# Optimization experiments

Hardware: AMD Instinct MI355X
Metric: run time of the kernel (lower is better)

## Reference

```python
import jax, jax.numpy as jnp
import numpy as np

B, T, D_IN, H, D = 4, 4096, 1024, 16, 64


def setup_inputs() -> dict:
    key = jax.random.key(0)
    k1, k2, k3 = jax.random.split(key, 3)
    inputs = jax.random.normal(k1, (B, T, D_IN), dtype=jnp.float32)
    kv_kernel = jax.random.normal(k2, (D_IN, H, D, 2), dtype=jnp.float32) * (1.0 / np.sqrt(D_IN))
    q_kernel = jax.random.normal(k3, (H, D), dtype=jnp.float32) * (1.0 / np.sqrt(D))
    return {"inputs": inputs, "kv_kernel": kv_kernel, "q_kernel": q_kernel}


def _associate(a, b):
    # Online-softmax combine on packed tuples [m(1), u(1), w(D)] along last axis.
    ma, ua, wa = a[..., :1], a[..., 1:2], a[..., 2:]
    mb, ub, wb = b[..., :1], b[..., 1:2], b[..., 2:]
    m = jnp.maximum(ma, mb)
    ea = jnp.exp(ma - m)
    eb = jnp.exp(mb - m)
    u = ua * ea + ub * eb
    w = wa * ea + wb * eb
    return jnp.concatenate([m, u, w], axis=-1)


def reference(inputs, kv_kernel, q_kernel):
    # inputs: (B,T,D_in); kv_kernel: (D_in,H,D,2); q_kernel: (H,D)
    kv = jnp.einsum('bti,ihdk->bthdk', inputs, kv_kernel)
    kv = jax.nn.relu(kv)  # activation; dropout disabled (inference)
    k = kv[..., 0]  # (B,T,H,D)
    v = kv[..., 1]  # (B,T,H,D)
    st = jnp.einsum('hd,bthd->bth', q_kernel, k)[..., None]  # (B,T,H,1)
    u_init = jnp.ones_like(st)  # exp(s - m) with m = s
    elems = jnp.concatenate([st, u_init, v], axis=-1)  # (B,T,H,D+2)
    o = jax.lax.associative_scan(_associate, elems, axis=1)
    c = o[..., 1:2]  # running denominator
    a = o[..., 2:]   # running numerator (B,T,H,D)
    h = a / c
    # concat_heads=False -> sum over heads
    return jnp.sum(h, axis=-2)  # (B,T,D)
```

## Files before the change

kernel.cpp:

```cpp
#include <hip/hip_runtime.h>
#include <hip/hip_bf16.h>
#include <math.h>

#define B_   4
#define T_   4096
#define DIN_ 1024
#define H_   16
#define D_   64
#define M_   (B_*T_)
#define N_   (H_*D_*2)
#define K_   DIN_
#define C_   64
#define CL_  (T_/C_)

typedef unsigned short u16;
typedef __attribute__((ext_vector_type(8))) short short8_t;
typedef __attribute__((ext_vector_type(4))) float float4_t;

__device__ __forceinline__ u16 f2bf(float f) {
  unsigned int x = __float_as_uint(f);
  x += 0x7fffu + ((x >> 16) & 1u);
  return (u16)(x >> 16);
}
__device__ __forceinline__ float bf2f(unsigned int u) {
  return __uint_as_float((u & 0xffffu) << 16);
}
__device__ __forceinline__ unsigned pk_bf16(float x, float y) {
  float2 f; f.x = x; f.y = y;
  union { __hip_bfloat162 h2; unsigned u; } c;
  c.h2 = __float22bfloat162_rn(f);
  return c.u;
}

__device__ __forceinline__ void g2l16(const u16* g, u16* l) {
  __builtin_amdgcn_global_load_lds(
      (const __attribute__((address_space(1))) void*)g,
      (__attribute__((address_space(3))) void*)l, 16, 0, 0);
}

__global__ __launch_bounds__(256)
void prep(const float* __restrict__ inputs, const float* __restrict__ kvk,
          u16* __restrict__ aB, u16* __restrict__ wBt) {
  __shared__ float tile[32][33];
  int bid = blockIdx.x;
  int tid = threadIdx.x;
  if (bid < 8192) {
    int i = bid * 256 + tid;
    const float4* src = (const float4*)inputs;
    float4 a = src[2*i], b = src[2*i+1];
    uint4 o;
    o.x = pk_bf16(a.x, a.y);
    o.y = pk_bf16(a.z, a.w);
    o.z = pk_bf16(b.x, b.y);
    o.w = pk_bf16(b.z, b.w);
    ((uint4*)aB)[i] = o;
  } else {
    int b2 = bid - 8192;
    int kb = (b2 & 31) * 32;
    int nb = (b2 >> 5) * 32;
    int r  = tid >> 3;
    int c4 = (tid & 7) * 4;
    float4 v = *(const float4*)&kvk[(size_t)(kb + r) * N_ + nb + c4];
    tile[r][c4+0] = v.x; tile[r][c4+1] = v.y; tile[r][c4+2] = v.z; tile[r][c4+3] = v.w;
    __syncthreads();
    uint2 o;
    o.x = pk_bf16(tile[c4+0][r], tile[c4+1][r]);
    o.y = pk_bf16(tile[c4+2][r], tile[c4+3][r]);
    *(uint2*)&wBt[(size_t)(nb + r) * K_ + kb + c4] = o;
  }
}


#define FENCE asm volatile("" ::: "memory")
#define KBAR do { FENCE; __builtin_amdgcn_s_barrier(); FENCE; } while (0)

#define STAGE_A(P, KT, CC) do { \
  g2l16(gA + ((size_t)((CC)*64      ) * K_ + (KT)*64), lds + (P)*16384 +        (CC)*4096 + wv*512); \
  g2l16(gA + ((size_t)((CC)*64 + 128) * K_ + (KT)*64), lds + (P)*16384 + 8192 + (CC)*4096 + wv*512); \
} while (0)

#define STAGE_B(P, KT, HH) do { \
  g2l16(gB + ((size_t)((HH)*128     ) * K_ + (KT)*64), lds + 32768 + (P)*16384 + (HH)*8192 +        wv*512); \
  g2l16(gB + ((size_t)((HH)*128 + 64) * K_ + (KT)*64), lds + 32768 + (P)*16384 + (HH)*8192 + 4096 + wv*512); \
} while (0)

#define READ_A(P, MH) do { _Pragma("unroll") \
  for (int il_ = 0; il_ < 4; ++il_) { \
    const int o_ = (P)*16384 + aBase + (MH)*4096 + il_*1024; \
    af[il_][0] = *(const short8_t*)&lds[o_ + s0]; \
    af[il_][1] = *(const short8_t*)&lds[o_ + s1]; \
  } } while (0)

#define READ_B(P, NH) do { _Pragma("unroll") \
  for (int jl_ = 0; jl_ < 2; ++jl_) { \
    const int o_ = (P)*16384 + (NH)*8192 + bBase + jl_*1024; \
    bfr[NH][jl_][0] = *(const short8_t*)&lds[o_ + s0]; \
    bfr[NH][jl_][1] = *(const short8_t*)&lds[o_ + s1]; \
  } } while (0)

#define MFMA_Q(MH, NH) do { \
  __builtin_amdgcn_s_setprio(1); \
  _Pragma("unroll") for (int kk_ = 0; kk_ < 2; ++kk_) \
  _Pragma("unroll") for (int il_ = 0; il_ < 4; ++il_) \
  _Pragma("unroll") for (int jl_ = 0; jl_ < 2; ++jl_) \
    acc[(MH)*4+il_][(NH)*2+jl_] = __builtin_amdgcn_mfma_f32_16x16x32_bf16( \
        af[il_][kk_], bfr[NH][jl_][kk_], acc[(MH)*4+il_][(NH)*2+jl_], 0, 0, 0); \
  __builtin_amdgcn_s_setprio(0); \
} while (0)

__global__ __launch_bounds__(512, 2)
void gemm_kv(const u16* __restrict__ A, const u16* __restrict__ Bt,
             const float* __restrict__ q,
             float* __restrict__ pbuf, u16* __restrict__ vbuf,
             float* __restrict__ aggU, float* __restrict__ aggW) {
  extern __shared__ __align__(16) char smem[];
  u16* lds = (u16*)smem;

  const int tid  = threadIdx.x;
  const int wv   = tid >> 6;
  const int lane = tid & 63;
  const int quad = lane >> 4;
  const int l16  = lane & 15;
  const int wr   = wv >> 2;
  const int wc   = wv & 3;

  const int g  = blockIdx.x;
  const int wg = (g & 7) * 64 + (g >> 3);
  const int nt = wg & 7;
  const int mt = wg >> 3;
  const int bm = mt * 256;
  const int bn = nt * 256;

  const int tr   = tid >> 3;
  const int gran = tid & 7;
  const u16* gA = A  + (size_t)(bm + tr) * K_ + ((gran ^ (tr & 7)) * 8);
  const u16* gB = Bt + (size_t)(bn + tr) * K_ + ((gran ^ (tr & 7)) * 8);

  const int s0 = ((quad    ) ^ (l16 & 7)) * 8;
  const int s1 = ((quad + 4) ^ (l16 & 7)) * 8;
  const int aBase = wr * 8192 + l16 * 64;
  const int bBase = 32768 + wc * 2048 + l16 * 64;

  float4_t acc[8][4] = {};
  short8_t af[4][2];
  short8_t bfr[2][2][2];

  STAGE_A(0, 0, 0); STAGE_A(0, 0, 1);
  STAGE_B(0, 0, 0); STAGE_B(0, 0, 1);
  STAGE_A(1, 1, 0); STAGE_B(1, 1, 0);
  asm volatile("s_waitcnt vmcnt(4)" ::: "memory");
  KBAR;

#pragma unroll 1
  for (int it = 0; it < 8; ++it) {
    const int kt1 = 2*it + 1, kt2 = 2*it + 2, kt3 = 2*it + 3;
    const bool more = (it < 7);
    READ_A(0, 0); READ_B(0, 0);
    STAGE_A(1, kt1, 1);
    KBAR;
    MFMA_Q(0, 0);
    KBAR;
    READ_B(0, 1);
    STAGE_B(1, kt1, 1);
    KBAR;
    MFMA_Q(0, 1);
    KBAR;
    READ_A(0, 1);
    if (more) STAGE_A(0, kt2, 0);
    KBAR;
    MFMA_Q(1, 0);
    KBAR;
    if (more) STAGE_B(0, kt2, 0);
    KBAR;
    MFMA_Q(1, 1);
    if (more) asm volatile("s_waitcnt vmcnt(4)" ::: "memory");
    else      asm volatile("s_waitcnt vmcnt(0)" ::: "memory");
    KBAR;
    READ_A(1, 0); READ_B(1, 0);
    if (more) STAGE_A(0, kt2, 1);
    KBAR;
    MFMA_Q(0, 0);
    KBAR;
    READ_B(1, 1);
    if (more) STAGE_B(0, kt2, 1);
    KBAR;
    MFMA_Q(0, 1);
    KBAR;
    READ_A(1, 1);
    if (more) STAGE_A(1, kt3, 0);
    KBAR;
    MFMA_Q(1, 0);
    KBAR;
    if (more) STAGE_B(1, kt3, 0);
    KBAR;
    MFMA_Q(1, 1);
    if (more) asm volatile("s_waitcnt vmcnt(4)" ::: "memory");
    KBAR;
  }

  u16*   vtile = (u16*)smem;
  float* sred  = (float*)(smem + 73728);
  float* pS    = (float*)(smem + 108544);

  float qv[2][2];
#pragma unroll
  for (int nh = 0; nh < 2; ++nh)
#pragma unroll
    for (int jl = 0; jl < 2; ++jl)
      qv[nh][jl] = q[nt*128 + nh*64 + wc*16 + jl*8 + (l16 >> 1)];

#pragma unroll
  for (int nh = 0; nh < 2; ++nh) {
#pragma unroll
    for (int i = 0; i < 8; ++i) {
#pragma unroll
      for (int r = 0; r < 4; ++r) {
        const int t = wr*128 + i*16 + quad*4 + r;
        const float x0 = fmaxf(acc[i][nh*2+0][r], 0.f);
        const float x1 = fmaxf(acc[i][nh*2+1][r], 0.f);
        if (l16 & 1) {
          const int d0 = (wc*32 + l16) >> 1;
          vtile[(nh*256 + t)*72 + d0    ] = f2bf(x0);
          vtile[(nh*256 + t)*72 + d0 + 8] = f2bf(x1);
        }
        float ps = qv[nh][0]*x0 + qv[nh][1]*x1;
        ps += __shfl_xor(ps, 2);
        if ((l16 & 3) == 0)
          sred[(nh*256 + t)*17 + wc*4 + (l16 >> 2)] = ps;
      }
    }
  }
  __syncthreads();

  const int b  = mt >> 4;
  const int t0 = (mt & 15) * 256;
  {
    const int hh = tid >> 8;
    const int t  = tid & 255;
    float s = 0.f;
#pragma unroll
    for (int k = 0; k < 16; ++k) s += sred[(hh*256 + t)*17 + k];
    float p = __expf(fminf(fmaxf(s, -60.f), 60.f));
    pS[hh*256 + t] = p;
    pbuf[(size_t)(b*H_ + nt*2 + hh) * T_ + t0 + t] = p;
    float u = p;
#pragma unroll
    for (int off = 32; off; off >>= 1) u += __shfl_down(u, off);
    if (lane == 0) {
      const int ch = (tid >> 6) & 3;
      aggU[(b*H_ + nt*2 + hh)*C_ + (mt & 15)*4 + ch] = u;
    }
  }
  __syncthreads();

  if (l16 & 1) {
    float Wv[2][2][2] = {};
#pragma unroll
    for (int nh = 0; nh < 2; ++nh)
#pragma unroll
      for (int i = 0; i < 8; ++i)
#pragma unroll
        for (int r = 0; r < 4; ++r) {
          const int t = wr*128 + i*16 + quad*4 + r;
          const float p = pS[nh*256 + t];
          Wv[nh][i>>2][0] += p * fmaxf(acc[i][nh*2+0][r], 0.f);
          Wv[nh][i>>2][1] += p * fmaxf(acc[i][nh*2+1][r], 0.f);
        }
#pragma unroll
    for (int nh = 0; nh < 2; ++nh)
#pragma unroll
      for (int c2 = 0; c2 < 2; ++c2)
#pragma unroll
        for (int jl = 0; jl < 2; ++jl) {
          float w = Wv[nh][c2][jl];
          w += __shfl_xor(w, 16);
          w += __shfl_xor(w, 32);
          if (quad == 0) {
            const int blk = (b*H_ + nt*2 + nh)*C_ + (mt & 15)*4 + wr*2 + c2;
            aggW[(size_t)blk * D_ + wc*16 + jl*8 + (l16 >> 1)] = w;
          }
        }
  }
  {
    const int rr = tid >> 3;
    const int d0 = (tid & 7) * 8;
#pragma unroll
    for (int k2 = 0; k2 < 8; ++k2) {
      const int row = rr + 64*k2;
      const int hh  = row >> 8;
      const int t   = row & 255;
      uint4 val = *(const uint4*)&vtile[(hh*256 + t)*72 + d0];
      *(uint4*)&vbuf[((size_t)(b*H_ + nt*2 + hh) * T_ + t0 + t) * D_ + d0] = val;
    }
  }
}

__global__ __launch_bounds__(1024)
void scan_pass3(const u16* __restrict__ vbuf, const float* __restrict__ pbuf,
                const float* __restrict__ aggU, const float* __restrict__ aggW,
                float* __restrict__ out) {
  __shared__ float pS[H_][CL_];
  __shared__ float wbuf[H_][8][D_ + 1];
  int bc = blockIdx.x;
  int b  = bc >> 6;
  int c  = bc & (C_ - 1);
  int tid  = threadIdx.x;
  int h    = tid >> 6;
  int lane = tid & 63;
  int bh   = b * H_ + h;
  int t0   = c * CL_;

  pS[h][lane] = pbuf[(size_t)bh * T_ + t0 + lane];

  float U = 0.f, W = 0.f;
  for (int j = 0; j < c; ++j) {
    int idx = bh * C_ + j;
    U += aggU[idx];
    W += aggW[(size_t)idx * D_ + lane];
  }
  __syncthreads();

  const u16* vp = vbuf + ((size_t)bh * T_ + t0) * D_ + lane;
  for (int gg = 0; gg < 8; ++gg) {
#pragma unroll
    for (int ii = 0; ii < 8; ++ii) {
      int i = gg * 8 + ii;
      float p = pS[h][i];
      float v = bf2f(vp[i * D_]);
      U += p;
      W += p * v;
      wbuf[h][ii][lane] = __fdividef(W, U);
    }
    __syncthreads();
    if (tid < 512) {
      int ii = tid >> 6, dd = tid & 63;
      float acc = 0.f;
#pragma unroll
      for (int hh = 0; hh < H_; ++hh) acc += wbuf[hh][ii][dd];
      out[((size_t)b * T_ + t0 + gg*8 + ii) * D_ + dd] = acc;
    }
    __syncthreads();
  }
}

extern "C" void kernel_launch(void* const* d_in, const int* in_sizes, int n_in,
                              void* d_out, int out_size, void* d_ws, size_t ws_size,
                              hipStream_t stream) {
  const float* inputs = (const float*)d_in[0];
  const float* kvk    = (const float*)d_in[1];
  const float* qk     = (const float*)d_in[2];
  float* out = (float*)d_out;
  char* ws = (char*)d_ws;

  u16*   aB   = (u16*)ws;
  u16*   wBt  = (u16*)(ws + 33554432);
  u16*   vb   = (u16*)(ws + 37748736);
  float* pb   = (float*)(ws + 71303168);
  float* aggU = (float*)(ws + 72351744);
  float* aggW = (float*)(ws + 72368128);

  prep<<<10240, 256, 0, stream>>>(inputs, kvk, aB, wBt);
  gemm_kv<<<2048 / 4, 512, 131072, stream>>>(aB, wBt, qk, pb, vb, aggU, aggW);
  scan_pass3<<<B_*C_, 1024, 0, stream>>>(vb, pb, aggU, aggW, out);
}
```

Baseline: 205.4 us.

## Restructure KV GEMM to 16 waves with K=32 triple-buffered LDS pipeline

Reworks the fused KV GEMM from 8 waves holding 128x64 register tiles, double-buffered with K=64 steps, to 16 waves per block each holding a 64x64 tile. The main loop now uses K=32 steps with a three-slot LDS ring and one stage per phase. LDS shrinks to 96KB and the launch becomes 1024 threads, and the epilogue is adapted to the new wave-to-tile mapping. The goal is more waves to hide latency and a simpler pipeline, at the cost of more barriers per unit of K and less register reuse per wave.

```diff
diff --git a/kernel.cpp b/kernel.cpp
--- a/kernel.cpp
+++ b/kernel.cpp
@@ -74,41 +74,35 @@
 #define FENCE asm volatile("" ::: "memory")
 #define KBAR do { FENCE; __builtin_amdgcn_s_barrier(); FENCE; } while (0)
 
-#define STAGE_A(P, KT, CC) do { \
-  g2l16(gA + ((size_t)((CC)*64      ) * K_ + (KT)*64), lds + (P)*16384 +        (CC)*4096 + wv*512); \
-  g2l16(gA + ((size_t)((CC)*64 + 128) * K_ + (KT)*64), lds + (P)*16384 + 8192 + (CC)*4096 + wv*512); \
+#define READS(PAR) do { _Pragma("unroll") \
+  for (int i_ = 0; i_ < 4; ++i_) \
+    af[i_] = *(const short8_t*)&lds[(PAR)*8192 + aBase + i_*512]; \
+  _Pragma("unroll") \
+  for (int j_ = 0; j_ < 4; ++j_) \
+    bfq[j_] = *(const short8_t*)&lds[(PAR)*8192 + bBase + j_*512]; \
 } while (0)
 
-#define STAGE_B(P, KT, HH) do { \
-  g2l16(gB + ((size_t)((HH)*128     ) * K_ + (KT)*64), lds + 32768 + (P)*16384 + (HH)*8192 +        wv*512); \
-  g2l16(gB + ((size_t)((HH)*128 + 64) * K_ + (KT)*64), lds + 32768 + (P)*16384 + (HH)*8192 + 4096 + wv*512); \
-} while (0)
-
-#define READ_A(P, MH) do { _Pragma("unroll") \
-  for (int il_ = 0; il_ < 4; ++il_) { \
-    const int o_ = (P)*16384 + aBase + (MH)*4096 + il_*1024; \
-    af[il_][0] = *(const short8_t*)&lds[o_ + s0]; \
-    af[il_][1] = *(const short8_t*)&lds[o_ + s1]; \
-  } } while (0)
-
-#define READ_B(P, NH) do { _Pragma("unroll") \
-  for (int jl_ = 0; jl_ < 2; ++jl_) { \
-    const int o_ = (P)*16384 + (NH)*8192 + bBase + jl_*1024; \
-    bfr[NH][jl_][0] = *(const short8_t*)&lds[o_ + s0]; \
-    bfr[NH][jl_][1] = *(const short8_t*)&lds[o_ + s1]; \
-  } } while (0)
-
-#define MFMA_Q(MH, NH) do { \
+#define MFMAS do { \
   __builtin_amdgcn_s_setprio(1); \
-  _Pragma("unroll") for (int kk_ = 0; kk_ < 2; ++kk_) \
-  _Pragma("unroll") for (int il_ = 0; il_ < 4; ++il_) \
-  _Pragma("unroll") for (int jl_ = 0; jl_ < 2; ++jl_) \
-    acc[(MH)*4+il_][(NH)*2+jl_] = __builtin_amdgcn_mfma_f32_16x16x32_bf16( \
-        af[il_][kk_], bfr[NH][jl_][kk_], acc[(MH)*4+il_][(NH)*2+jl_], 0, 0, 0); \
+  _Pragma("unroll") for (int i_ = 0; i_ < 4; ++i_) \
+  _Pragma("unroll") for (int j_ = 0; j_ < 4; ++j_) \
+    acc[i_][j_] = __builtin_amdgcn_mfma_f32_16x16x32_bf16( \
+        af[i_], bfq[j_], acc[i_][j_], 0, 0, 0); \
   __builtin_amdgcn_s_setprio(0); \
 } while (0)
 
-__global__ __launch_bounds__(512, 2)
+#define PHASE(PAR, PAR2, KT) do { \
+  short8_t af[4], bfq[4]; \
+  READS(PAR); \
+  g2l16(gA + ((KT)+2)*32, lds +         (PAR2)*8192 + wv*512); \
+  g2l16(gB + ((KT)+2)*32, lds + 24576 + (PAR2)*8192 + wv*512); \
+  KBAR; \
+  MFMAS; \
+  asm volatile("s_waitcnt vmcnt(2)" ::: "memory"); \
+  KBAR; \
+} while (0)
+
+__global__ __launch_bounds__(1024)
 void gemm_kv(const u16* __restrict__ A, const u16* __restrict__ Bt,
              const float* __restrict__ q,
              float* __restrict__ pbuf, u16* __restrict__ vbuf,
@@ -121,8 +115,8 @@
   const int lane = tid & 63;
   const int quad = lane >> 4;
   const int l16  = lane & 15;
-  const int wr   = wv >> 2;
-  const int wc   = wv & 3;
+  const int wr2  = wv >> 2;
+  const int wc2  = wv & 3;
 
   const int g  = blockIdx.x;
   const int wg = (g & 7) * 64 + (g >> 3);
@@ -131,102 +125,78 @@
   const int bm = mt * 256;
   const int bn = nt * 256;
 
-  const int tr   = tid >> 3;
-  const int gran = tid & 7;
-  const u16* gA = A  + (size_t)(bm + tr) * K_ + ((gran ^ (tr & 7)) * 8);
-  const u16* gB = Bt + (size_t)(bn + tr) * K_ + ((gran ^ (tr & 7)) * 8);
-
-  const int s0 = ((quad    ) ^ (l16 & 7)) * 8;
-  const int s1 = ((quad + 4) ^ (l16 & 7)) * 8;
-  const int aBase = wr * 8192 + l16 * 64;
-  const int bBase = 32768 + wc * 2048 + l16 * 64;
-
-  float4_t acc[8][4] = {};
-  short8_t af[4][2];
-  short8_t bfr[2][2][2];
-
-  STAGE_A(0, 0, 0); STAGE_A(0, 0, 1);
-  STAGE_B(0, 0, 0); STAGE_B(0, 0, 1);
-  STAGE_A(1, 1, 0); STAGE_B(1, 1, 0);
-  asm volatile("s_waitcnt vmcnt(4)" ::: "memory");
+  const u16* gA = A  + (size_t)(bm + (tid >> 2)) * K_ + (((tid & 3) ^ ((tid >> 3) & 3)) * 8);
+  const u16* gB = Bt + (size_t)(bn + (tid >> 2)) * K_ + (((tid & 3) ^ ((tid >> 3) & 3)) * 8);
+
+  const int sg    = (quad ^ ((l16 >> 1) & 3)) * 8;
+  const int aBase = wr2 * 2048 + l16 * 32 + sg;
+  const int bBase = 24576 + wc2 * 2048 + l16 * 32 + sg;
+
+  float4_t acc[4][4] = {};
+
+  g2l16(gA,      lds +                 wv*512);
+  g2l16(gB,      lds + 24576 +         wv*512);
+  g2l16(gA + 32, lds +          8192 + wv*512);
+  g2l16(gB + 32, lds + 24576 +  8192 + wv*512);
+  asm volatile("s_waitcnt vmcnt(2)" ::: "memory");
   KBAR;
 
 #pragma unroll 1
-  for (int it = 0; it < 8; ++it) {
-    const int kt1 = 2*it + 1, kt2 = 2*it + 2, kt3 = 2*it + 3;
-    const bool more = (it < 7);
-    READ_A(0, 0); READ_B(0, 0);
-    STAGE_A(1, kt1, 1);
+  for (int kq = 0; kq < 10; ++kq) {
+    const int kt = kq * 3;
+    PHASE(0, 2, kt + 0);
+    PHASE(1, 0, kt + 1);
+    PHASE(2, 1, kt + 2);
+  }
+  {
+    short8_t af[4], bfq[4];
+    READS(0);
     KBAR;
-    MFMA_Q(0, 0);
+    MFMAS;
+    asm volatile("s_waitcnt vmcnt(0)" ::: "memory");
     KBAR;
-    READ_B(0, 1);
-    STAGE_B(1, kt1, 1);
+  }
+  {
+    short8_t af[4], bfq[4];
+    READS(1);
     KBAR;
-    MFMA_Q(0, 1);
-    KBAR;
-    READ_A(0, 1);
-    if (more) STAGE_A(0, kt2, 0);
-    KBAR;
-    MFMA_Q(1, 0);
-    KBAR;
-    if (more) STAGE_B(0, kt2, 0);
-    KBAR;
-    MFMA_Q(1, 1);
-    if (more) asm volatile("s_waitcnt vmcnt(4)" ::: "memory");
-    else      asm volatile("s_waitcnt vmcnt(0)" ::: "memory");
-    KBAR;
-    READ_A(1, 0); READ_B(1, 0);
-    if (more) STAGE_A(0, kt2, 1);
-    KBAR;
-    MFMA_Q(0, 0);
-    KBAR;
-    READ_B(1, 1);
-    if (more) STAGE_B(0, kt2, 1);
-    KBAR;
-    MFMA_Q(0, 1);
-    KBAR;
-    READ_A(1, 1);
-    if (more) STAGE_A(1, kt3, 0);
-    KBAR;
-    MFMA_Q(1, 0);
-    KBAR;
-    if (more) STAGE_B(1, kt3, 0);
-    KBAR;
-    MFMA_Q(1, 1);
-    if (more) asm volatile("s_waitcnt vmcnt(4)" ::: "memory");
+    MFMAS;
     KBAR;
   }
 
   u16*   vtile = (u16*)smem;
   float* sred  = (float*)(smem + 73728);
-  float* pS    = (float*)(smem + 108544);
-
-  float qv[2][2];
-#pragma unroll
-  for (int nh = 0; nh < 2; ++nh)
-#pragma unroll
-    for (int jl = 0; jl < 2; ++jl)
-      qv[nh][jl] = q[nt*128 + nh*64 + wc*16 + jl*8 + (l16 >> 1)];
-
-#pragma unroll
-  for (int nh = 0; nh < 2; ++nh) {
-#pragma unroll
-    for (int i = 0; i < 8; ++i) {
-#pragma unroll
-      for (int r = 0; r < 4; ++r) {
-        const int t = wr*128 + i*16 + quad*4 + r;
-        const float x0 = fmaxf(acc[i][nh*2+0][r], 0.f);
-        const float x1 = fmaxf(acc[i][nh*2+1][r], 0.f);
-        if (l16 & 1) {
-          const int d0 = (wc*32 + l16) >> 1;
-          vtile[(nh*256 + t)*72 + d0    ] = f2bf(x0);
-          vtile[(nh*256 + t)*72 + d0 + 8] = f2bf(x1);
-        }
-        float ps = qv[nh][0]*x0 + qv[nh][1]*x1;
+  float* pS    = (float*)(smem + 83968);
+
+  const int nh   = wc2 >> 1;
+  const int wc2p = wc2 & 1;
+  const int hd   = l16 >> 1;
+
+  float qv[4];
+#pragma unroll
+  for (int j = 0; j < 4; ++j)
+    qv[j] = q[(nt*2 + nh)*64 + wc2p*32 + j*8 + hd];
+
+#pragma unroll
+  for (int i = 0; i < 4; ++i) {
+#pragma unroll
+    for (int r = 0; r < 4; ++r) {
+      const int t = wr2*64 + i*16 + quad*4 + r;
+      float x0 = fmaxf(acc[i][0][r], 0.f);
+      float x1 = fmaxf(acc[i][1][r], 0.f);
+      float x2 = fmaxf(acc[i][2][r], 0.f);
+      float x3 = fmaxf(acc[i][3][r], 0.f);
+      if (l16 & 1) {
+        vtile[(nh*256 + t)*72 + wc2p*32 +  0 + hd] = f2bf(x0);
+        vtile[(nh*256 + t)*72 + wc2p*32 +  8 + hd] = f2bf(x1);
+        vtile[(nh*256 + t)*72 + wc2p*32 + 16 + hd] = f2bf(x2);
+        vtile[(nh*256 + t)*72 + wc2p*32 + 24 + hd] = f2bf(x3);
+      } else {
+        float ps = qv[0]*x0 + qv[1]*x1 + qv[2]*x2 + qv[3]*x3;
         ps += __shfl_xor(ps, 2);
-        if ((l16 & 3) == 0)
-          sred[(nh*256 + t)*17 + wc*4 + (l16 >> 2)] = ps;
+        ps += __shfl_xor(ps, 4);
+        if ((l16 & 7) == 0)
+          sred[(nh*256 + t)*5 + wc2p*2 + (l16 >> 3)] = ps;
       }
     }
   }
@@ -234,59 +204,51 @@
 
   const int b  = mt >> 4;
   const int t0 = (mt & 15) * 256;
-  {
+  if (tid < 512) {
     const int hh = tid >> 8;
     const int t  = tid & 255;
-    float s = 0.f;
-#pragma unroll
-    for (int k = 0; k < 16; ++k) s += sred[(hh*256 + t)*17 + k];
+    const float* sr = &sred[(hh*256 + t)*5];
+    float s = sr[0] + sr[1] + sr[2] + sr[3];
     float p = __expf(fminf(fmaxf(s, -60.f), 60.f));
     pS[hh*256 + t] = p;
     pbuf[(size_t)(b*H_ + nt*2 + hh) * T_ + t0 + t] = p;
     float u = p;
 #pragma unroll
     for (int off = 32; off; off >>= 1) u += __shfl_down(u, off);
-    if (lane == 0) {
-      const int ch = (tid >> 6) & 3;
-      aggU[(b*H_ + nt*2 + hh)*C_ + (mt & 15)*4 + ch] = u;
-    }
+    if (lane == 0)
+      aggU[(b*H_ + nt*2 + hh)*C_ + (mt & 15)*4 + ((tid >> 6) & 3)] = u;
   }
   __syncthreads();
 
   if (l16 & 1) {
-    float Wv[2][2][2] = {};
-#pragma unroll
-    for (int nh = 0; nh < 2; ++nh)
-#pragma unroll
-      for (int i = 0; i < 8; ++i)
-#pragma unroll
-        for (int r = 0; r < 4; ++r) {
-          const int t = wr*128 + i*16 + quad*4 + r;
-          const float p = pS[nh*256 + t];
-          Wv[nh][i>>2][0] += p * fmaxf(acc[i][nh*2+0][r], 0.f);
-          Wv[nh][i>>2][1] += p * fmaxf(acc[i][nh*2+1][r], 0.f);
-        }
-#pragma unroll
-    for (int nh = 0; nh < 2; ++nh)
-#pragma unroll
-      for (int c2 = 0; c2 < 2; ++c2)
-#pragma unroll
-        for (int jl = 0; jl < 2; ++jl) {
-          float w = Wv[nh][c2][jl];
-          w += __shfl_xor(w, 16);
-          w += __shfl_xor(w, 32);
-          if (quad == 0) {
-            const int blk = (b*H_ + nt*2 + nh)*C_ + (mt & 15)*4 + wr*2 + c2;
-            aggW[(size_t)blk * D_ + wc*16 + jl*8 + (l16 >> 1)] = w;
-          }
-        }
+    float Wv[4] = {};
+#pragma unroll
+    for (int i = 0; i < 4; ++i)
+#pragma unroll
+      for (int r = 0; r < 4; ++r) {
+        const int t = wr2*64 + i*16 + quad*4 + r;
+        const float p = pS[nh*256 + t];
+        Wv[0] += p * fmaxf(acc[i][0][r], 0.f);
+        Wv[1] += p * fmaxf(acc[i][1][r], 0.f);
+        Wv[2] += p * fmaxf(acc[i][2][r], 0.f);
+        Wv[3] += p * fmaxf(acc[i][3][r], 0.f);
+      }
+#pragma unroll
+    for (int j = 0; j < 4; ++j) {
+      float w = Wv[j];
+      w += __shfl_xor(w, 16);
+      w += __shfl_xor(w, 32);
+      if (quad == 0) {
+        const int blk = (b*H_ + nt*2 + nh)*C_ + (mt & 15)*4 + wr2;
+        aggW[(size_t)blk * D_ + wc2p*32 + j*8 + hd] = w;
+      }
+    }
   }
   {
-    const int rr = tid >> 3;
     const int d0 = (tid & 7) * 8;
 #pragma unroll
-    for (int k2 = 0; k2 < 8; ++k2) {
-      const int row = rr + 64*k2;
+    for (int k2 = 0; k2 < 4; ++k2) {
+      const int row = (tid >> 3) + 128*k2;
       const int hh  = row >> 8;
       const int t   = row & 255;
       uint4 val = *(const uint4*)&vtile[(hh*256 + t)*72 + d0];
@@ -360,6 +322,6 @@
   float* aggW = (float*)(ws + 72368128);
 
   prep<<<10240, 256, 0, stream>>>(inputs, kvk, aB, wBt);
-  gemm_kv<<<2048 / 4, 512, 131072, stream>>>(aB, wBt, qk, pb, vb, aggU, aggW);
+  gemm_kv<<<512, 1024, 98304, stream>>>(aB, wBt, qk, pb, vb, aggU, aggW);
   scan_pass3<<<B_*C_, 1024, 0, stream>>>(vb, pb, aggU, aggW, out);
 }
```

Result: no change. 202.5 us, median of 2 (-1.4%).
